# Performance work log

Hardware: AMD Instinct MI355X
Metric: run time of the kernel (lower is better)

The kernel has to match this reference:

```python
import jax, jax.numpy as jnp
import numpy as np

EPS = 1e-10


def setup_inputs() -> dict:
    key = jax.random.key(0)
    k1, k2 = jax.random.split(key)
    B, C, H, W = 8, 16, 256, 256
    x = jax.random.normal(k1, (B, C, H, W), dtype=jnp.float32)
    # grid_sample-style normalized coords in [-1, 1]
    inv_grid = jax.random.uniform(k2, (B, H, W, 2), dtype=jnp.float32, minval=-1.0, maxval=1.0)
    return {"x": x, "inv_grid": inv_grid}


def reference(x, inv_grid):
    B, C, Hin, Win = x.shape
    h, w = Hin, Win  # OH = OW = None -> output size equals input size

    g = (inv_grid + 1.0) * 0.5
    # coord 0 scaled by h, coord 1 by w, shifted by +1 (padding row/col), clamped
    ci = jnp.clip(g[..., 0] * h + 1.0, 0.0, h + 1 - 2 * EPS)
    cj = jnp.clip(g[..., 1] * w + 1.0, 0.0, w + 1 - 2 * EPS)
    i0 = jnp.floor(ci).astype(jnp.int32)  # coords >= 0 so floor == trunc (.long())
    j0 = jnp.floor(cj).astype(jnp.int32)

    # broadcast over channel dim (grid is shared across channels)
    ci_ = ci[:, None]
    cj_ = cj[:, None]
    i0_ = i0[:, None]
    j0_ = j0[:, None]

    bidx = jnp.arange(B)[:, None, None, None]
    cidx = jnp.arange(C)[None, :, None, None]

    A = jnp.zeros((B, C, h + 3, w + 3), dtype=x.dtype)
    for di in range(2):
        wi = jax.nn.relu(1.0 - jnp.abs(ci_ - (i0_ + di).astype(ci_.dtype)))
        for dj in range(2):
            wj = jax.nn.relu(1.0 - jnp.abs(cj_ - (j0_ + dj).astype(cj_.dtype)))
            # bilinear splat scatter-add of x * weight into the 4 corner cells
            A = A.at[bidx, cidx, i0_ + di, j0_ + dj].add(x * (wi * wj))
    return A[..., 1:h + 1, 1:w + 1]
```

## Files before the change

kernel.cpp:

```cpp
#include <hip/hip_runtime.h>
#include <hip/hip_fp16.h>
#include <stdint.h>

#define BB 8
#define CC 16
#define HH 256
#define WW 256
#define HW (HH * WW)
#define NSRC (BB * HW)
#define NBLK (NSRC / 256)
#define MAXSLOT 15
#define REC_DW 12
#define CNT_BYTES ((size_t)NSRC * 4)


__global__ __launch_bounds__(256) void pass1_bin(
    const float* __restrict__ inv_grid,
    uint32_t* __restrict__ counts,
    uint32_t* __restrict__ srcmeta,
    uint32_t* __restrict__ fifj)
{
    const int idx = blockIdx.x * 256 + threadIdx.x;
    const float2 g2 = ((const float2*)inv_grid)[idx];
    const float ci = fminf(fmaxf(fmaf((g2.x + 1.0f) * 0.5f, (float)HH, 1.0f), 0.0f), 257.0f);
    const float cj = fminf(fmaxf(fmaf((g2.y + 1.0f) * 0.5f, (float)WW, 1.0f), 0.0f), 257.0f);
    const int i0 = (int)floorf(ci);
    const int j0 = (int)floorf(cj);
    const float fi = ci - (float)i0;
    const float fj = cj - (float)j0;
    const int bi = i0 - 1, bj = j0 - 1;
    uint32_t meta = 0xFFFFFFFFu;
    if (((unsigned)bi < HH) & ((unsigned)bj < WW)) {
        const int b = idx >> 16;
        const uint32_t bin = (b << 16) | (bi << 8) | bj;
        const uint32_t slot = atomicAdd(&counts[bin], 1u);
        if (slot < MAXSLOT) meta = (bin << 4) | slot;
    }
    srcmeta[idx] = meta;
    const uint32_t fi16 = (uint32_t)(fi * 65535.0f + 0.5f);
    const uint32_t fj16 = (uint32_t)(fj * 65535.0f + 0.5f);
    fifj[idx] = fi16 | (fj16 << 16);
}

__global__ __launch_bounds__(256) void scanA(
    const uint32_t* __restrict__ counts,
    uint32_t* __restrict__ offsets,
    uint32_t* __restrict__ bsum)
{
    __shared__ uint32_t s[256];
    const int t = threadIdx.x;
    const int i = blockIdx.x * 256 + t;
    const uint32_t v = counts[i];
    s[t] = v;
    __syncthreads();
#pragma unroll
    for (int d = 1; d < 256; d <<= 1) {
        const uint32_t u = (t >= d) ? s[t - d] : 0u;
        __syncthreads();
        s[t] += u;
        __syncthreads();
    }
    offsets[i] = s[t] - v;
    if (t == 255) bsum[blockIdx.x] = s[255];
}

__global__ __launch_bounds__(1024) void scanB(uint32_t* __restrict__ bsum)
{
    __shared__ uint32_t s[1024];
    const int t = threadIdx.x;
    const uint32_t a  = bsum[2 * t];
    const uint32_t b2 = bsum[2 * t + 1];
    const uint32_t pair = a + b2;
    s[t] = pair;
    __syncthreads();
#pragma unroll
    for (int d = 1; d < 1024; d <<= 1) {
        const uint32_t u = (t >= d) ? s[t - d] : 0u;
        __syncthreads();
        s[t] += u;
        __syncthreads();
    }
    const uint32_t excl = s[t] - pair;
    bsum[2 * t]     = excl;
    bsum[2 * t + 1] = excl + a;
}

__global__ __launch_bounds__(256) void fill_records(
    const float* __restrict__ x,
    const uint32_t* __restrict__ srcmeta,
    const uint32_t* __restrict__ fifj,
    const uint32_t* __restrict__ offsets,
    const uint32_t* __restrict__ bsum,
    uint32_t* __restrict__ records)
{
    const int idx = blockIdx.x * 256 + threadIdx.x;
    const uint32_t meta = srcmeta[idx];
    if (meta == 0xFFFFFFFFu) return;
    const uint32_t bin  = meta >> 4;
    const uint32_t slot = meta & 15u;
    const uint32_t pos  = offsets[bin] + bsum[bin >> 8] + slot;

    const int b = idx >> 16;
    const int p = idx & 0xFFFF;
    const float* xp = x + (((size_t)b * CC) << 16) + p;

    uint32_t h[8];
#pragma unroll
    for (int q = 0; q < 8; ++q) {
        const float v0 = xp[(size_t)(2 * q)     << 16];
        const float v1 = xp[(size_t)(2 * q + 1) << 16];
        const uint32_t h0 = (uint32_t)__half_as_ushort(__float2half_rn(v0));
        const uint32_t h1 = (uint32_t)__half_as_ushort(__float2half_rn(v1));
        h[q] = h0 | (h1 << 16);
    }
    uint4 q0; q0.x = h[0]; q0.y = h[1]; q0.z = h[2]; q0.w = h[3];
    uint4 q1; q1.x = h[4]; q1.y = h[5]; q1.z = h[6]; q1.w = h[7];
    uint4* r4 = (uint4*)records;
    r4[(size_t)pos * 3]     = q0;
    r4[(size_t)pos * 3 + 1] = q1;
    records[(size_t)pos * REC_DW + 8] = fifj[idx];
}

__global__ __launch_bounds__(256) void gather_csr(
    const uint32_t* __restrict__ counts,
    const uint32_t* __restrict__ offsets,
    const uint32_t* __restrict__ bsum,
    const uint32_t* __restrict__ records,
    float* __restrict__ out)
{
    const int g   = blockIdx.x;
    const int b   = g & 7;
    const int seq = g >> 3;
    const int r   = ((seq >> 4) << 4) + (threadIdx.x >> 4);
    const int c   = ((seq & 15) << 4) + (threadIdx.x & 15);

    float acc[CC];
#pragma unroll
    for (int q = 0; q < CC; ++q) acc[q] = 0.0f;

    const uint4* r4 = (const uint4*)records;

#pragma unroll
    for (int di = 0; di < 2; ++di) {
        const int i0c = r + di;
        if (i0c < 1) continue;
#pragma unroll
        for (int dj = 0; dj < 2; ++dj) {
            const int j0c = c + dj;
            if (j0c < 1) continue;
            const uint32_t bin = (b << 16) | ((i0c - 1) << 8) | (j0c - 1);
            uint32_t cnt = counts[bin];
            if (cnt > MAXSLOT) cnt = MAXSLOT;
            const uint32_t off = offsets[bin] + bsum[bin >> 8];
            for (uint32_t k = 0; k < cnt; ++k) {
                const size_t pos = (size_t)(off + k);
                const uint32_t f2 = records[pos * REC_DW + 8];
                const float fi = (float)(f2 & 0xFFFFu) * (1.0f / 65535.0f);
                const float fj = (float)(f2 >> 16)     * (1.0f / 65535.0f);
                const float wi = di ? (1.0f - fi) : fi;
                const float wj = dj ? (1.0f - fj) : fj;
                const float w = wi * wj;
                const uint4 q0 = r4[pos * 3];
                const uint4 q1 = r4[pos * 3 + 1];
                const uint32_t hs[8] = {q0.x, q0.y, q0.z, q0.w, q1.x, q1.y, q1.z, q1.w};
#pragma unroll
                for (int q = 0; q < 8; ++q) {
                    const float v0 = __half2float(__ushort_as_half((unsigned short)(hs[q] & 0xFFFFu)));
                    const float v1 = __half2float(__ushort_as_half((unsigned short)(hs[q] >> 16)));
                    acc[2 * q]     += w * v0;
                    acc[2 * q + 1] += w * v1;
                }
            }
        }
    }

    float* op = out + (((size_t)(b * CC)) << 16) + (r << 8) + c;
#pragma unroll
    for (int q = 0; q < CC; ++q)
        op[(size_t)q << 16] = acc[q];
}

__global__ __launch_bounds__(256) void invgrid_scatter_direct(
    const float* __restrict__ x,
    const float* __restrict__ inv_grid,
    float* __restrict__ out)
{
    const int idx = blockIdx.x * 256 + threadIdx.x;
    const int b = idx >> 16;
    const float2 g2 = ((const float2*)inv_grid)[idx];
    const float ci = fminf(fmaxf(fmaf((g2.x + 1.0f) * 0.5f, (float)HH, 1.0f), 0.0f), 257.0f);
    const float cj = fminf(fmaxf(fmaf((g2.y + 1.0f) * 0.5f, (float)WW, 1.0f), 0.0f), 257.0f);
    const int i0 = (int)floorf(ci);
    const int j0 = (int)floorf(cj);
    const float wi0 = fmaxf(0.0f, 1.0f - fabsf(ci - (float)i0));
    const float wi1 = fmaxf(0.0f, 1.0f - fabsf(ci - (float)(i0 + 1)));
    const float wj0 = fmaxf(0.0f, 1.0f - fabsf(cj - (float)j0));
    const float wj1 = fmaxf(0.0f, 1.0f - fabsf(cj - (float)(j0 + 1)));
    const float w00 = wi0 * wj0, w01 = wi0 * wj1;
    const float w10 = wi1 * wj0, w11 = wi1 * wj1;
    const int r0 = i0 - 1, r1 = i0, c0 = j0 - 1, c1 = j0;
    const bool vr0 = (unsigned)r0 < HH, vr1 = (unsigned)r1 < HH;
    const bool vc0 = (unsigned)c0 < WW, vc1 = (unsigned)c1 < WW;
    const int o00 = r0 * WW + c0, o01 = r0 * WW + c1;
    const int o10 = r1 * WW + c0, o11 = r1 * WW + c1;
    const int p = idx & 0xFFFF;
    const float* xp = x + (size_t)b * CC * HW + p;
    float* op = out + (size_t)b * CC * HW;
#pragma unroll
    for (int cch = 0; cch < CC; ++cch) {
        const float xv = xp[(size_t)cch * HW];
        float* ob = op + (size_t)cch * HW;
        if (vr0 & vc0) atomicAdd(ob + o00, xv * w00);
        if (vr0 & vc1) atomicAdd(ob + o01, xv * w01);
        if (vr1 & vc0) atomicAdd(ob + o10, xv * w10);
        if (vr1 & vc1) atomicAdd(ob + o11, xv * w11);
    }
}

extern "C" void kernel_launch(void* const* d_in, const int* in_sizes, int n_in,
                              void* d_out, int out_size, void* d_ws, size_t ws_size,
                              hipStream_t stream) {
    const float* x        = (const float*)d_in[0];
    const float* inv_grid = (const float*)d_in[1];
    float* out            = (float*)d_out;

    const size_t A = 256;
    size_t o_counts  = 0;
    size_t o_offsets = o_counts  + (CNT_BYTES + A - 1) / A * A;
    size_t o_bsum    = o_offsets + (CNT_BYTES + A - 1) / A * A;
    size_t o_srcmeta = o_bsum    + ((size_t)NBLK * 4 + A - 1) / A * A;
    size_t o_fifj    = o_srcmeta + (CNT_BYTES + A - 1) / A * A;
    size_t o_records = o_fifj    + (CNT_BYTES + A - 1) / A * A;
    size_t csr_need  = o_records + (size_t)NSRC * REC_DW * 4;

    if (ws_size >= csr_need) {
        char* w = (char*)d_ws;
        uint32_t* counts  = (uint32_t*)(w + o_counts);
        uint32_t* offsets = (uint32_t*)(w + o_offsets);
        uint32_t* bsum    = (uint32_t*)(w + o_bsum);
        uint32_t* srcmeta = (uint32_t*)(w + o_srcmeta);
        uint32_t* fifj    = (uint32_t*)(w + o_fifj);
        uint32_t* records = (uint32_t*)(w + o_records);
        hipMemsetAsync(counts, 0, CNT_BYTES, stream);
        pass1_bin   <<<NBLK, 256,  0, stream>>>(inv_grid, counts, srcmeta, fifj);
        scanA       <<<NBLK, 256,  0, stream>>>(counts, offsets, bsum);
        scanB       <<<1,    1024, 0, stream>>>(bsum);
        fill_records<<<NBLK, 256,  0, stream>>>(x, srcmeta, fifj, offsets, bsum, records);
        gather_csr  <<<NBLK, 256,  0, stream>>>(counts, offsets, bsum, records, out);
    } else {
        hipMemsetAsync(d_out, 0, (size_t)out_size * sizeof(float), stream);
        invgrid_scatter_direct<<<NBLK, 256, 0, stream>>>(x, inv_grid, out);
    }
}
```

Before: 152.9 us.

## Split CSR records into separate fraction and fp16 payload arrays, pack count/offset pairs

```diff
diff --git a/kernel.cpp b/kernel.cpp
--- a/kernel.cpp
+++ b/kernel.cpp
@@ -10,15 +10,13 @@
 #define NSRC (BB * HW)
 #define NBLK (NSRC / 256)
 #define MAXSLOT 15
-#define REC_DW 12
 #define CNT_BYTES ((size_t)NSRC * 4)
 
 
 __global__ __launch_bounds__(256) void pass1_bin(
     const float* __restrict__ inv_grid,
     uint32_t* __restrict__ counts,
-    uint32_t* __restrict__ srcmeta,
-    uint32_t* __restrict__ fifj)
+    uint2* __restrict__ srcs)
 {
     const int idx = blockIdx.x * 256 + threadIdx.x;
     const float2 g2 = ((const float2*)inv_grid)[idx];
@@ -36,15 +34,15 @@
         const uint32_t slot = atomicAdd(&counts[bin], 1u);
         if (slot < MAXSLOT) meta = (bin << 4) | slot;
     }
-    srcmeta[idx] = meta;
     const uint32_t fi16 = (uint32_t)(fi * 65535.0f + 0.5f);
     const uint32_t fj16 = (uint32_t)(fj * 65535.0f + 0.5f);
-    fifj[idx] = fi16 | (fj16 << 16);
+    uint2 m; m.x = meta; m.y = fi16 | (fj16 << 16);
+    srcs[idx] = m;
 }
 
 __global__ __launch_bounds__(256) void scanA(
     const uint32_t* __restrict__ counts,
-    uint32_t* __restrict__ offsets,
+    uint2* __restrict__ co,
     uint32_t* __restrict__ bsum)
 {
     __shared__ uint32_t s[256];
@@ -60,7 +58,8 @@
         s[t] += u;
         __syncthreads();
     }
-    offsets[i] = s[t] - v;
+    uint2 e; e.x = v; e.y = s[t] - v;
+    co[i] = e;
     if (t == 255) bsum[blockIdx.x] = s[255];
 }
 
@@ -87,18 +86,18 @@
 
 __global__ __launch_bounds__(256) void fill_records(
     const float* __restrict__ x,
-    const uint32_t* __restrict__ srcmeta,
-    const uint32_t* __restrict__ fifj,
-    const uint32_t* __restrict__ offsets,
+    const uint2* __restrict__ srcs,
+    const uint2* __restrict__ co,
     const uint32_t* __restrict__ bsum,
-    uint32_t* __restrict__ records)
+    uint32_t* __restrict__ ff,
+    uint4* __restrict__ pl)
 {
     const int idx = blockIdx.x * 256 + threadIdx.x;
-    const uint32_t meta = srcmeta[idx];
-    if (meta == 0xFFFFFFFFu) return;
-    const uint32_t bin  = meta >> 4;
-    const uint32_t slot = meta & 15u;
-    const uint32_t pos  = offsets[bin] + bsum[bin >> 8] + slot;
+    const uint2 m = srcs[idx];
+    if (m.x == 0xFFFFFFFFu) return;
+    const uint32_t bin  = m.x >> 4;
+    const uint32_t slot = m.x & 15u;
+    const uint32_t pos  = co[bin].y + bsum[bin >> 8] + slot;
 
     const int b = idx >> 16;
     const int p = idx & 0xFFFF;
@@ -113,19 +112,18 @@
         const uint32_t h1 = (uint32_t)__half_as_ushort(__float2half_rn(v1));
         h[q] = h0 | (h1 << 16);
     }
+    ff[pos] = m.y;
     uint4 q0; q0.x = h[0]; q0.y = h[1]; q0.z = h[2]; q0.w = h[3];
     uint4 q1; q1.x = h[4]; q1.y = h[5]; q1.z = h[6]; q1.w = h[7];
-    uint4* r4 = (uint4*)records;
-    r4[(size_t)pos * 3]     = q0;
-    r4[(size_t)pos * 3 + 1] = q1;
-    records[(size_t)pos * REC_DW + 8] = fifj[idx];
+    pl[(size_t)pos * 2]     = q0;
+    pl[(size_t)pos * 2 + 1] = q1;
 }
 
 __global__ __launch_bounds__(256) void gather_csr(
-    const uint32_t* __restrict__ counts,
-    const uint32_t* __restrict__ offsets,
+    const uint2* __restrict__ co,
     const uint32_t* __restrict__ bsum,
-    const uint32_t* __restrict__ records,
+    const uint32_t* __restrict__ ff,
+    const uint4* __restrict__ pl,
     float* __restrict__ out)
 {
     const int g   = blockIdx.x;
@@ -138,8 +136,6 @@
 #pragma unroll
     for (int q = 0; q < CC; ++q) acc[q] = 0.0f;
 
-    const uint4* r4 = (const uint4*)records;
-
 #pragma unroll
     for (int di = 0; di < 2; ++di) {
         const int i0c = r + di;
@@ -149,19 +145,20 @@
             const int j0c = c + dj;
             if (j0c < 1) continue;
             const uint32_t bin = (b << 16) | ((i0c - 1) << 8) | (j0c - 1);
-            uint32_t cnt = counts[bin];
+            const uint2 e = co[bin];
+            uint32_t cnt = e.x;
             if (cnt > MAXSLOT) cnt = MAXSLOT;
-            const uint32_t off = offsets[bin] + bsum[bin >> 8];
+            const uint32_t off = e.y + bsum[bin >> 8];
             for (uint32_t k = 0; k < cnt; ++k) {
                 const size_t pos = (size_t)(off + k);
-                const uint32_t f2 = records[pos * REC_DW + 8];
+                const uint32_t f2 = ff[pos];
                 const float fi = (float)(f2 & 0xFFFFu) * (1.0f / 65535.0f);
                 const float fj = (float)(f2 >> 16)     * (1.0f / 65535.0f);
                 const float wi = di ? (1.0f - fi) : fi;
                 const float wj = dj ? (1.0f - fj) : fj;
                 const float w = wi * wj;
-                const uint4 q0 = r4[pos * 3];
-                const uint4 q1 = r4[pos * 3 + 1];
+                const uint4 q0 = pl[pos * 2];
+                const uint4 q1 = pl[pos * 2 + 1];
                 const uint32_t hs[8] = {q0.x, q0.y, q0.z, q0.w, q1.x, q1.y, q1.z, q1.w};
 #pragma unroll
                 for (int q = 0; q < 8; ++q) {
@@ -225,28 +222,28 @@
     float* out            = (float*)d_out;
 
     const size_t A = 256;
-    size_t o_counts  = 0;
-    size_t o_offsets = o_counts  + (CNT_BYTES + A - 1) / A * A;
-    size_t o_bsum    = o_offsets + (CNT_BYTES + A - 1) / A * A;
-    size_t o_srcmeta = o_bsum    + ((size_t)NBLK * 4 + A - 1) / A * A;
-    size_t o_fifj    = o_srcmeta + (CNT_BYTES + A - 1) / A * A;
-    size_t o_records = o_fifj    + (CNT_BYTES + A - 1) / A * A;
-    size_t csr_need  = o_records + (size_t)NSRC * REC_DW * 4;
-
-    if (ws_size >= csr_need) {
+    size_t o_counts = 0;
+    size_t o_co     = o_counts + (CNT_BYTES + A - 1) / A * A;
+    size_t o_bsum   = o_co     + ((size_t)NSRC * 8 + A - 1) / A * A;
+    size_t o_srcs   = o_bsum   + ((size_t)NBLK * 4 + A - 1) / A * A;
+    size_t o_ff     = o_srcs   + ((size_t)NSRC * 8 + A - 1) / A * A;
+    size_t o_pl     = o_ff     + (CNT_BYTES + A - 1) / A * A;
+    size_t need     = o_pl     + (size_t)NSRC * 32;
+
+    if (ws_size >= need) {
         char* w = (char*)d_ws;
-        uint32_t* counts  = (uint32_t*)(w + o_counts);
-        uint32_t* offsets = (uint32_t*)(w + o_offsets);
-        uint32_t* bsum    = (uint32_t*)(w + o_bsum);
-        uint32_t* srcmeta = (uint32_t*)(w + o_srcmeta);
-        uint32_t* fifj    = (uint32_t*)(w + o_fifj);
-        uint32_t* records = (uint32_t*)(w + o_records);
+        uint32_t* counts = (uint32_t*)(w + o_counts);
+        uint2*    co     = (uint2*)   (w + o_co);
+        uint32_t* bsum   = (uint32_t*)(w + o_bsum);
+        uint2*    srcs   = (uint2*)   (w + o_srcs);
+        uint32_t* ff     = (uint32_t*)(w + o_ff);
+        uint4*    pl     = (uint4*)   (w + o_pl);
         hipMemsetAsync(counts, 0, CNT_BYTES, stream);
-        pass1_bin   <<<NBLK, 256,  0, stream>>>(inv_grid, counts, srcmeta, fifj);
-        scanA       <<<NBLK, 256,  0, stream>>>(counts, offsets, bsum);
+        pass1_bin   <<<NBLK, 256,  0, stream>>>(inv_grid, counts, srcs);
+        scanA       <<<NBLK, 256,  0, stream>>>(counts, co, bsum);
         scanB       <<<1,    1024, 0, stream>>>(bsum);
-        fill_records<<<NBLK, 256,  0, stream>>>(x, srcmeta, fifj, offsets, bsum, records);
-        gather_csr  <<<NBLK, 256,  0, stream>>>(counts, offsets, bsum, records, out);
+        fill_records<<<NBLK, 256,  0, stream>>>(x, srcs, co, bsum, ff, pl);
+        gather_csr  <<<NBLK, 256,  0, stream>>>(co, bsum, ff, pl, out);
     } else {
         hipMemsetAsync(d_out, 0, (size_t)out_size * sizeof(float), stream);
         invgrid_scatter_direct<<<NBLK, 256, 0, stream>>>(x, inv_grid, out);
```

Measured after the change: 149.0 us (median of 2 runs). 1.03x faster.
